# Kernel optimization log

Hardware: AMD Instinct MI355X
Metric: run time of the kernel (lower is better)

## Reference

```python
import jax, jax.numpy as jnp
import numpy as np
import math

HEADS = 32
DIM_HEAD = 64
DM = HEADS * DIM_HEAD  # 2048
B, S = 2, 1024
BITS = 3
N_LEVELS = 2 ** BITS
N_GROUPS = (DIM_HEAD + 2) // 3  # 22
PAD = (3 - DIM_HEAD % 3) % 3    # 2
EPS_NORM = 1e-8
EPS_RMS = 1e-6


def _rotors_to_matrices(r):
    # r: (G,4) unit rotors [s, b12, b13, b23] -> (G,3,3) rotation matrices
    s, p, q, rr = r[:, 0], r[:, 1], r[:, 2], r[:, 3]
    s2, p2, q2, r2 = s * s, p * p, q * q, rr * rr
    M = np.zeros((r.shape[0], 3, 3), dtype=np.float32)
    M[:, 0, 0] = s2 - p2 - q2 + r2
    M[:, 0, 1] = 2 * s * p - 2 * q * rr
    M[:, 0, 2] = 2 * s * q + 2 * p * rr
    M[:, 1, 0] = -2 * s * p - 2 * q * rr
    M[:, 1, 1] = s2 - p2 + q2 - r2
    M[:, 1, 2] = 2 * s * rr - 2 * p * q
    M[:, 2, 0] = -2 * s * q + 2 * p * rr
    M[:, 2, 1] = -2 * s * rr - 2 * p * q
    M[:, 2, 2] = s2 + p2 - q2 - r2
    return M


def _make_compressor(seed):
    rng = np.random.default_rng(seed)
    rot = rng.standard_normal((N_GROUPS, 4)).astype(np.float32)
    rot /= np.linalg.norm(rot, axis=-1, keepdims=True)
    M = _rotors_to_matrices(rot)
    sigma = 1.0 / math.sqrt(DIM_HEAD)  # Lloyd-Max for N(0, 1/d)
    C = np.linspace(-3 * sigma, 3 * sigma, N_LEVELS, dtype=np.float32)
    return jnp.asarray(M), jnp.asarray(np.ascontiguousarray(M.transpose(0, 2, 1))), jnp.asarray(C)


def setup_inputs() -> dict:
    key = jax.random.key(0)
    ks = jax.random.split(key, 8)
    x = jax.random.normal(ks[0], (B, S, DM), dtype=jnp.float32)
    w_scale = 0.02
    Wq = jax.random.normal(ks[1], (DM, DM), dtype=jnp.float32) * w_scale
    Wk = jax.random.normal(ks[2], (DM, DM), dtype=jnp.float32) * w_scale
    Wv = jax.random.normal(ks[3], (DM, DM), dtype=jnp.float32) * w_scale
    Wo = jax.random.normal(ks[4], (DM, DM), dtype=jnp.float32) * w_scale
    qn_w = jnp.ones((DM,), dtype=jnp.float32)
    kn_w = jnp.ones((DM,), dtype=jnp.float32)
    Mk, Mtk, Ck = _make_compressor(42)
    Mv, Mtv, Cv = _make_compressor(4200)
    return {"x": x, "Wq": Wq, "Wk": Wk, "Wv": Wv, "Wo": Wo,
            "qn_w": qn_w, "kn_w": kn_w,
            "Mk": Mk, "Mtk": Mtk, "Ck": Ck,
            "Mv": Mv, "Mtv": Mtv, "Cv": Cv}


def _rmsnorm(x, w):
    return x * jax.lax.rsqrt(jnp.mean(x * x, axis=-1, keepdims=True) + EPS_RMS) * w


def _quant_roundtrip(h, M, Mt, C):
    """RotorQuant compress+decompress. h: (B,H,S,Dh) -> (B,H,S,Dh)."""
    norms = jnp.maximum(jnp.linalg.norm(h, axis=-1, keepdims=True), EPS_NORM)
    xu = h / norms
    xu = jnp.pad(xu, ((0, 0), (0, 0), (0, 0), (0, PAD)))
    g = xu.reshape(h.shape[0], h.shape[1], h.shape[2], N_GROUPS, 3)
    rot = jnp.einsum('bhsgi,gij->bhsgj', g, M)
    flat = rot.reshape(h.shape[0], h.shape[1], h.shape[2], N_GROUPS * 3)
    # nearest-centroid quantization (uint8 indices in original)
    idx = jnp.argmin(jnp.abs(flat[..., None] - C), axis=-1)
    deq = C[idx]
    g2 = deq.reshape(h.shape[0], h.shape[1], h.shape[2], N_GROUPS, 3)
    der = jnp.einsum('bhsgi,gij->bhsgj', g2, Mt)
    out = der.reshape(h.shape[0], h.shape[1], h.shape[2], N_GROUPS * 3)[..., :DIM_HEAD]
    return out * norms


def reference(x, Wq, Wk, Wv, Wo, qn_w, kn_w, Mk, Mtk, Ck, Mv, Mtv, Cv):
    b, s, _ = x.shape
    v = x @ Wv
    q = _rmsnorm(x @ Wq, qn_w)
    k = _rmsnorm(x @ Wk, kn_w)
    # split heads -> (B,H,S,Dh)
    qh = q.reshape(b, s, HEADS, DIM_HEAD).transpose(0, 2, 1, 3)
    kh = k.reshape(b, s, HEADS, DIM_HEAD).transpose(0, 2, 1, 3)
    vh = v.reshape(b, s, HEADS, DIM_HEAD).transpose(0, 2, 1, 3)
    # per-head rotor quantization roundtrip of K and V
    kh = _quant_roundtrip(kh, Mk, Mtk, Ck)
    vh = _quant_roundtrip(vh, Mv, Mtv, Cv)
    # scaled dot-product attention
    scores = jnp.einsum('bhqd,bhkd->bhqk', qh, kh) / math.sqrt(DIM_HEAD)
    probs = jax.nn.softmax(scores, axis=-1)
    o = jnp.einsum('bhqk,bhkd->bhqd', probs, vh)
    o = o.transpose(0, 2, 1, 3).reshape(b, s, DM)
    return o @ Wo
```

## Files before the change

### kernel.cpp

```cpp
#include <hip/hip_runtime.h>
#include <hip/hip_bf16.h>
#include <math.h>

#define HEADS 32
#define DIM_HEAD 64
#define DM 2048
#define BATCH 2
#define SEQ 1024
#define NROWS (BATCH * SEQ)
#define NVEC (NROWS * HEADS)
#define N_GROUPS 22
#define N_LEVELS 8
#define EPS_NORM 1e-8f
#define EPS_RMS 1e-6f

typedef float f32x4 __attribute__((ext_vector_type(4)));
typedef __bf16 bf16x8 __attribute__((ext_vector_type(8)));
typedef unsigned short u16x8 __attribute__((ext_vector_type(8)));
typedef unsigned short u16x4 __attribute__((ext_vector_type(4)));

__device__ __forceinline__ unsigned short f2bf(float x) {
  union { float f; unsigned u; } v; v.f = x;
  unsigned r = v.u + 0x7fffu + ((v.u >> 16) & 1u);
  return (unsigned short)(r >> 16);
}
__device__ __forceinline__ float bf2f(unsigned short h) {
  union { unsigned u; float f; } v; v.u = ((unsigned)h) << 16;
  return v.f;
}
__device__ __forceinline__ bf16x8 ldfrag(const unsigned short* p) {
  return __builtin_bit_cast(bf16x8, *(const u16x8*)p);
}
#define MFMA16(a, b, c) __builtin_amdgcn_mfma_f32_16x16x32_bf16((a), (b), (c), 0, 0, 0)

__device__ __forceinline__ void stage16(const unsigned short* g, unsigned short* lds) {
  __builtin_amdgcn_global_load_lds(
      (const __attribute__((address_space(1))) unsigned int*)g,
      (__attribute__((address_space(3))) unsigned int*)lds, 16, 0, 0);
}

#define WAITV(N) asm volatile("s_waitcnt vmcnt(" #N ")" ::: "memory")
#define SBARM()  asm volatile("s_barrier" ::: "memory")
#define SFENCE() __builtin_amdgcn_sched_barrier(0)

__global__ __launch_bounds__(256) void split_convert_kernel(
    const float* __restrict__ X, unsigned short* __restrict__ hi,
    unsigned short* __restrict__ lo, int n8) {
  const int i = blockIdx.x * 256 + threadIdx.x;
  if (i >= n8) return;
  const float4 a = ((const float4*)X)[2 * i];
  const float4 b = ((const float4*)X)[2 * i + 1];
  const float v[8] = {a.x, a.y, a.z, a.w, b.x, b.y, b.z, b.w};
  u16x8 h, l;
#pragma unroll
  for (int j = 0; j < 8; ++j) {
    const unsigned short hh = f2bf(v[j]);
    h[j] = hh;
    l[j] = f2bf(v[j] - bf2f(hh));
  }
  ((u16x8*)hi)[i] = h;
  if (lo) ((u16x8*)lo)[i] = l;
}

__global__ __launch_bounds__(256) void transpose_split_batch_kernel(
    const float* __restrict__ W0, const float* __restrict__ W1,
    const float* __restrict__ W2, const float* __restrict__ W3,
    unsigned short* __restrict__ T0h, unsigned short* __restrict__ T1h,
    unsigned short* __restrict__ T1l, unsigned short* __restrict__ T2h,
    unsigned short* __restrict__ T2l, unsigned short* __restrict__ T3h) {
  const int z = blockIdx.z;
  const float* W = (z == 0) ? W0 : (z == 1) ? W1 : (z == 2) ? W2 : W3;
  unsigned short* Th = (z == 0) ? T0h : (z == 1) ? T1h : (z == 2) ? T2h : T3h;
  unsigned short* Tl = (z == 1) ? T1l : (z == 2) ? T2l : nullptr;

  __shared__ float S[64][65];
  const int t = threadIdx.x;
  const int tk = blockIdx.y * 64, tm = blockIdx.x * 64;
  {
    const int r = t >> 2, cs = (t & 3) * 16;
    const float* src = W + (size_t)(tk + r) * DM + tm + cs;
#pragma unroll
    for (int j = 0; j < 16; j += 4) {
      float4 v = *(const float4*)(src + j);
      S[r][cs + j] = v.x; S[r][cs + j + 1] = v.y;
      S[r][cs + j + 2] = v.z; S[r][cs + j + 3] = v.w;
    }
  }
  __syncthreads();
  const int m = t >> 2, ks = (t & 3) * 16;
  u16x8 h0, h1, l0, l1;
#pragma unroll
  for (int j = 0; j < 8; ++j) {
    const float v = S[ks + j][m];
    const unsigned short hh = f2bf(v);
    h0[j] = hh; l0[j] = f2bf(v - bf2f(hh));
  }
#pragma unroll
  for (int j = 0; j < 8; ++j) {
    const float v = S[ks + 8 + j][m];
    const unsigned short hh = f2bf(v);
    h1[j] = hh; l1[j] = f2bf(v - bf2f(hh));
  }
  const size_t o = (size_t)(tm + m) * DM + tk + ks;
  *(u16x8*)&Th[o] = h0; *(u16x8*)&Th[o + 8] = h1;
  if (Tl) { *(u16x8*)&Tl[o] = l0; *(u16x8*)&Tl[o + 8] = l1; }
}

__global__ __launch_bounds__(256) void qkv_gemm_kernel(
    const unsigned short* __restrict__ Ahi, const unsigned short* __restrict__ Alo,
    const unsigned short* __restrict__ Bhi, const unsigned short* __restrict__ Blo,
    float* __restrict__ q, float* __restrict__ k, float* __restrict__ v) {
  __shared__ unsigned short lAhi[128 * 32];
  __shared__ unsigned short lBhi[128 * 32];
  __shared__ unsigned short lAlo[128 * 32];
  __shared__ unsigned short lBlo[128 * 32];

  const int t = threadIdx.x;
  const int lane = t & 63, wave = t >> 6;
  const int wr = wave >> 1, wc = wave & 1;
  const int gm0 = blockIdx.y * 128;
  const int gnc = blockIdx.x * 128;
  const int seg = gnc >> 11;
  const bool split = (seg != 0);
  const int lrsub = lane >> 2;
  const int lcsub = lane & 3;

  f32x4 acc[4][4] = {};

  for (int kt = 0; kt < DM; kt += 32) {
    __syncthreads();
#pragma unroll
    for (int rg = wave; rg < 8; rg += 4) {
      const int lrow = rg * 16 + lrsub;
      const int c = lcsub ^ ((lrow >> 1) & 3);
      const size_t goffA = (size_t)(gm0 + lrow) * DM + kt + c * 8;
      const size_t goffB = (size_t)(gnc + lrow) * DM + kt + c * 8;
      stage16(Ahi + goffA, lAhi + rg * 512);
      stage16(Bhi + goffB, lBhi + rg * 512);
      if (split) {
        stage16(Alo + goffA, lAlo + rg * 512);
        stage16(Blo + goffB, lBlo + rg * 512);
      }
    }
    __syncthreads();

    bf16x8 ah[4], bh[4], al[4], bl[4];
#pragma unroll
    for (int i = 0; i < 4; ++i) {
      const int mrow = wr * 64 + i * 16 + (lane & 15);
      const int offa = mrow * 32 + (((lane >> 4) ^ ((mrow >> 1) & 3)) << 3);
      ah[i] = ldfrag(&lAhi[offa]);
      const int nrow = wc * 64 + i * 16 + (lane & 15);
      const int offb = nrow * 32 + (((lane >> 4) ^ ((nrow >> 1) & 3)) << 3);
      bh[i] = ldfrag(&lBhi[offb]);
      if (split) {
        al[i] = ldfrag(&lAlo[offa]);
        bl[i] = ldfrag(&lBlo[offb]);
      }
    }
#pragma unroll
    for (int i = 0; i < 4; ++i)
#pragma unroll
      for (int j = 0; j < 4; ++j) {
        acc[i][j] = MFMA16(ah[i], bh[j], acc[i][j]);
        if (split) {
          acc[i][j] = MFMA16(ah[i], bl[j], acc[i][j]);
          acc[i][j] = MFMA16(al[i], bh[j], acc[i][j]);
        }
      }
  }

  float* C = (seg == 0) ? q : (seg == 1) ? k : v;
  const int gn0 = gnc & 2047;
#pragma unroll
  for (int i = 0; i < 4; ++i) {
    const int row = gm0 + wr * 64 + i * 16 + ((lane >> 4) << 2);
#pragma unroll
    for (int j = 0; j < 4; ++j) {
      const int col = gn0 + wc * 64 + j * 16 + (lane & 15);
#pragma unroll
      for (int r = 0; r < 4; ++r)
        C[(size_t)(row + r) * DM + col] = acc[i][j][r];
    }
  }
}

__global__ __launch_bounds__(256) void gemm_out_splitk_kernel(
    const unsigned short* __restrict__ Ahi, const unsigned short* __restrict__ Bt,
    float* __restrict__ Cpart) {
  __shared__ unsigned short lAhi[128 * 32];
  __shared__ unsigned short lBhi[128 * 32];

  const int t = threadIdx.x;
  const int lane = t & 63, wave = t >> 6;
  const int wr = wave >> 1, wc = wave & 1;
  const int gm0 = blockIdx.y * 128, gn0 = blockIdx.x * 128;
  const int z = blockIdx.z;
  const int k0 = z * (DM / 2);
  const int lrsub = lane >> 2;
  const int lcsub = lane & 3;

  f32x4 acc[4][4] = {};

  for (int kt = k0; kt < k0 + DM / 2; kt += 32) {
    __syncthreads();
#pragma unroll
    for (int rg = wave; rg < 8; rg += 4) {
      const int lrow = rg * 16 + lrsub;
      const int c = lcsub ^ ((lrow >> 1) & 3);
      stage16(Ahi + (size_t)(gm0 + lrow) * DM + kt + c * 8, lAhi + rg * 512);
      stage16(Bt + (size_t)(gn0 + lrow) * DM + kt + c * 8, lBhi + rg * 512);
    }
    __syncthreads();

    bf16x8 ah[4], bh[4];
#pragma unroll
    for (int i = 0; i < 4; ++i) {
      const int mrow = wr * 64 + i * 16 + (lane & 15);
      ah[i] = ldfrag(&lAhi[mrow * 32 + (((lane >> 4) ^ ((mrow >> 1) & 3)) << 3)]);
      const int nrow = wc * 64 + i * 16 + (lane & 15);
      bh[i] = ldfrag(&lBhi[nrow * 32 + (((lane >> 4) ^ ((nrow >> 1) & 3)) << 3)]);
    }
#pragma unroll
    for (int i = 0; i < 4; ++i)
#pragma unroll
      for (int j = 0; j < 4; ++j)
        acc[i][j] = MFMA16(ah[i], bh[j], acc[i][j]);
  }

  float* C = Cpart + (size_t)z * NROWS * DM;
#pragma unroll
  for (int i = 0; i < 4; ++i) {
    const int row = gm0 + wr * 64 + i * 16 + ((lane >> 4) << 2);
#pragma unroll
    for (int j = 0; j < 4; ++j) {
      const int col = gn0 + wc * 64 + j * 16 + (lane & 15);
#pragma unroll
      for (int r = 0; r < 4; ++r)
        C[(size_t)(row + r) * DM + col] = acc[i][j][r];
    }
  }
}

__global__ __launch_bounds__(256) void add2_f4_kernel(
    const float* __restrict__ a, const float* __restrict__ b,
    float* __restrict__ o, int n4) {
  const int i = blockIdx.x * 256 + threadIdx.x;
  if (i >= n4) return;
  const float4 x = ((const float4*)a)[i];
  const float4 y = ((const float4*)b)[i];
  ((float4*)o)[i] = make_float4(x.x + y.x, x.y + y.y, x.z + y.z, x.w + y.w);
}

__device__ __forceinline__ float wave_sum(float x) {
#pragma unroll
  for (int o = 32; o > 0; o >>= 1) x += __shfl_xor(x, o, 64);
  return x;
}

__global__ __launch_bounds__(256) void rmsnorm_kernel(
    float* __restrict__ y, const float* __restrict__ w) {
  __shared__ float rbuf[4];
  const int row = blockIdx.x;
  float* p = y + (size_t)row * DM;
  const int t = threadIdx.x;
  const int wave = t >> 6, lane = t & 63;

  float ss = 0.f;
#pragma unroll
  for (int c = t; c < DM; c += 256) { float v = p[c]; ss += v * v; }
  ss = wave_sum(ss);
  if (lane == 0) rbuf[wave] = ss;
  __syncthreads();
  ss = rbuf[0] + rbuf[1] + rbuf[2] + rbuf[3];
  const float scale = rsqrtf(ss * (1.0f / DM) + EPS_RMS);
#pragma unroll
  for (int c = t; c < DM; c += 256) p[c] = p[c] * scale * w[c];
}

__global__ __launch_bounds__(256) void rmsnorm_split_kernel(
    const float* __restrict__ y, const float* __restrict__ w,
    unsigned short* __restrict__ hi, unsigned short* __restrict__ lo,
    float post) {
  __shared__ float rbuf[4];
  const int row = blockIdx.x;
  const float* p = y + (size_t)row * DM;
  const int t = threadIdx.x;
  const int wave = t >> 6, lane = t & 63;

  const int c0 = t * 8;
  float4 a = *(const float4*)(p + c0);
  float4 b = *(const float4*)(p + c0 + 4);
  float v[8] = {a.x, a.y, a.z, a.w, b.x, b.y, b.z, b.w};
  float ss = 0.f;
#pragma unroll
  for (int j = 0; j < 8; ++j) ss += v[j] * v[j];
  ss = wave_sum(ss);
  if (lane == 0) rbuf[wave] = ss;
  __syncthreads();
  ss = rbuf[0] + rbuf[1] + rbuf[2] + rbuf[3];
  const float scale = rsqrtf(ss * (1.0f / DM) + EPS_RMS) * post;

  u16x8 hv, lv;
#pragma unroll
  for (int j = 0; j < 8; ++j) {
    const float val = v[j] * scale * w[c0 + j];
    const unsigned short hh = f2bf(val);
    hv[j] = hh; lv[j] = f2bf(val - bf2f(hh));
  }
  *(u16x8*)&hi[(size_t)row * DM + c0] = hv;
  *(u16x8*)&lo[(size_t)row * DM + c0] = lv;
}

__device__ __forceinline__ float qnearest(float v, const float* __restrict__ C) {
  float best = C[0];
  float bd = fabsf(v - C[0]);
#pragma unroll
  for (int i = 1; i < N_LEVELS; ++i) {
    float d = fabsf(v - C[i]);
    if (d < bd) { bd = d; best = C[i]; }
  }
  return best;
}

template <bool WRITE_BF>
__global__ __launch_bounds__(256) void quant_kernel(
    float* __restrict__ kv, const float* __restrict__ M,
    const float* __restrict__ Mt, const float* __restrict__ C,
    unsigned short* __restrict__ hi, unsigned short* __restrict__ lo) {
  const int vec = blockIdx.x * blockDim.x + threadIdx.x;
  if (vec >= NVEC) return;
  float* p = kv + (size_t)vec * DIM_HEAD;

  float h[66];
  float ss = 0.f;
#pragma unroll
  for (int d = 0; d < DIM_HEAD; ++d) { h[d] = p[d]; ss += h[d] * h[d]; }
  float norm = fmaxf(sqrtf(ss), EPS_NORM);
  const float inv = 1.0f / norm;
#pragma unroll
  for (int d = 0; d < DIM_HEAD; ++d) h[d] *= inv;
  h[64] = 0.f; h[65] = 0.f;

#pragma unroll
  for (int g = 0; g < N_GROUPS; ++g) {
    const float* Mg  = M  + g * 9;
    const float* Mtg = Mt + g * 9;
    const float a0 = h[3 * g + 0], a1 = h[3 * g + 1], a2 = h[3 * g + 2];
    const float r0 = a0 * Mg[0] + a1 * Mg[3] + a2 * Mg[6];
    const float r1 = a0 * Mg[1] + a1 * Mg[4] + a2 * Mg[7];
    const float r2 = a0 * Mg[2] + a1 * Mg[5] + a2 * Mg[8];
    const float d0 = qnearest(r0, C);
    const float d1 = qnearest(r1, C);
    const float d2 = qnearest(r2, C);
    h[3 * g + 0] = d0 * Mtg[0] + d1 * Mtg[3] + d2 * Mtg[6];
    h[3 * g + 1] = d0 * Mtg[1] + d1 * Mtg[4] + d2 * Mtg[7];
    h[3 * g + 2] = d0 * Mtg[2] + d1 * Mtg[5] + d2 * Mtg[8];
  }
  if (WRITE_BF) {
#pragma unroll
    for (int g8 = 0; g8 < 8; ++g8) {
      u16x8 hv, lv;
#pragma unroll
      for (int j = 0; j < 8; ++j) {
        const float val = h[g8 * 8 + j] * norm;
        const unsigned short hh = f2bf(val);
        hv[j] = hh; lv[j] = f2bf(val - bf2f(hh));
      }
      *(u16x8*)&hi[(size_t)vec * DIM_HEAD + g8 * 8] = hv;
      *(u16x8*)&lo[(size_t)vec * DIM_HEAD + g8 * 8] = lv;
    }
  } else {
#pragma unroll
    for (int d = 0; d < DIM_HEAD; ++d) p[d] = h[d] * norm;
  }
}

__global__ __launch_bounds__(256) void vt_split_kernel(
    const float* __restrict__ v, unsigned short* __restrict__ hi,
    unsigned short* __restrict__ lo) {
  __shared__ float T[64][65];
  const int s0 = blockIdx.x * 64;
  const int bh = blockIdx.y;
  const int b = bh >> 5, h = bh & 31;
  const int t = threadIdx.x;
  {
    const int sr = t >> 2, dseg = (t & 3) * 16;
    const float* src = v + ((size_t)(b * SEQ + s0 + sr) * DM + h * 64 + dseg);
#pragma unroll
    for (int j = 0; j < 16; j += 4) {
      float4 a = *(const float4*)(src + j);
      T[sr][dseg + j] = a.x; T[sr][dseg + j + 1] = a.y;
      T[sr][dseg + j + 2] = a.z; T[sr][dseg + j + 3] = a.w;
    }
  }
  __syncthreads();
  const int d = t >> 2, sseg = (t & 3) * 16;
  u16x8 h0, h1, l0, l1;
#pragma unroll
  for (int j = 0; j < 8; ++j) {
    const float val = T[sseg + j][d];
    const unsigned short hh = f2bf(val);
    h0[j] = hh; l0[j] = f2bf(val - bf2f(hh));
  }
#pragma unroll
  for (int j = 0; j < 8; ++j) {
    const float val = T[sseg + 8 + j][d];
    const unsigned short hh = f2bf(val);
    h1[j] = hh; l1[j] = f2bf(val - bf2f(hh));
  }
  const size_t o = (size_t)(bh * 64 + d) * SEQ + s0 + sseg;
  *(u16x8*)&hi[o] = h0; *(u16x8*)&hi[o + 8] = h1;
  *(u16x8*)&lo[o] = l0; *(u16x8*)&lo[o + 8] = l1;
}

__global__ __launch_bounds__(256) void attn_mfma_kernel(
    const unsigned short* __restrict__ qhi, const unsigned short* __restrict__ qlo,
    const unsigned short* __restrict__ khi, const unsigned short* __restrict__ klo,
    const unsigned short* __restrict__ vthi, const unsigned short* __restrict__ vtlo,
    unsigned short* __restrict__ ohi) {
  __shared__ unsigned short Ks_h[2][4096], Ks_l[2][4096];
  __shared__ unsigned short Vt_h[2][4096], Vt_l[2][4096];
  __shared__ unsigned int   Ps[4096];

  const int bh = blockIdx.x;
  const int qt = blockIdx.y;
  const int h = bh & 31, b = bh >> 5;
  const int q0 = qt * 64;
  const int t = threadIdx.x, lane = t & 63, w = t >> 6;
  const int quad = lane >> 4, l15 = lane & 15;
  const int srow = lane >> 3, schunk = lane & 7;

  auto stage = [&](const unsigned short* g, int stride, unsigned short* arr) {
#pragma unroll
    for (int it = 0; it < 2; ++it) {
      const int r = w * 16 + it * 8 + srow;
      const int c = schunk ^ (r & 7);
      stage16(g + (size_t)r * stride + c * 8, arr + (w * 16 + it * 8) * 64);
    }
  };

  const unsigned short* gkh = khi + ((size_t)(b * SEQ) * DM + h * 64);
  const unsigned short* gkl = klo + ((size_t)(b * SEQ) * DM + h * 64);
  const unsigned short* gvh = vthi + (size_t)(bh * 64) * SEQ;
  const unsigned short* gvl = vtlo + (size_t)(bh * 64) * SEQ;

  auto stageAll = [&](int kt, int buf) {
    stage(gkh + (size_t)kt * DM, DM, Ks_h[buf]);
    stage(gkl + (size_t)kt * DM, DM, Ks_l[buf]);
    stage(gvh + kt, SEQ, Vt_h[buf]);
    stage(gvl + kt, SEQ, Vt_l[buf]);
  };

  bf16x8 qh[2], ql[2];
  {
    const size_t qrow = (size_t)(b * SEQ + q0 + w * 16 + l15) * DM + h * 64;
#pragma unroll
    for (int ks = 0; ks < 2; ++ks) {
      qh[ks] = ldfrag(&qhi[qrow + ks * 32 + quad * 8]);
      ql[ks] = ldfrag(&qlo[qrow + ks * 32 + quad * 8]);
    }
  }

  f32x4 acc[4] = {};
  float m_prev[4] = {-INFINITY, -INFINITY, -INFINITY, -INFINITY};
  float lsum[4] = {0.f, 0.f, 0.f, 0.f};

  stageAll(0, 0);

  for (int tt = 0; tt < 16; ++tt) {
    const int c = tt & 1, n = c ^ 1;
    if (tt < 15) {
      stageAll((tt + 1) * 64, n);
      WAITV(8);
    } else {
      WAITV(0);
    }
    SBARM(); SFENCE();
    const unsigned short* cKh = Ks_h[c];
    const unsigned short* cKl = Ks_l[c];
    const unsigned short* cVh = Vt_h[c];
    const unsigned short* cVl = Vt_l[c];

    f32x4 s[4] = {};
    __builtin_amdgcn_s_setprio(1);
#pragma unroll
    for (int nt = 0; nt < 4; ++nt) {
#pragma unroll
      for (int ks = 0; ks < 2; ++ks) {
        const int row = nt * 16 + l15;
        const int off = row * 64 + (((quad + 4 * ks) ^ (row & 7)) << 3);
        const bf16x8 kh = ldfrag(&cKh[off]);
        const bf16x8 kl = ldfrag(&cKl[off]);
        s[nt] = MFMA16(qh[ks], kh, s[nt]);
        s[nt] = MFMA16(qh[ks], kl, s[nt]);
        s[nt] = MFMA16(ql[ks], kh, s[nt]);
      }
    }
    __builtin_amdgcn_s_setprio(0);

    float asave[4];
#pragma unroll
    for (int r = 0; r < 4; ++r) {
      float mx = fmaxf(fmaxf(s[0][r], s[1][r]), fmaxf(s[2][r], s[3][r]));
#pragma unroll
      for (int off = 1; off < 16; off <<= 1) mx = fmaxf(mx, __shfl_xor(mx, off, 64));
      const float mn = fmaxf(m_prev[r], mx);
      const float al = __expf(m_prev[r] - mn);
      float rs = 0.f;
#pragma unroll
      for (int nt = 0; nt < 4; ++nt) {
        const float e = __expf(s[nt][r] - mn);
        s[nt][r] = e; rs += e;
      }
#pragma unroll
      for (int off = 1; off < 16; off <<= 1) rs += __shfl_xor(rs, off, 64);
      lsum[r] = lsum[r] * al + rs;
      m_prev[r] = mn;
      asave[r] = al;
      const int prow = w * 16 + quad * 4 + r;
#pragma unroll
      for (int nt = 0; nt < 4; ++nt) {
        const int kk = nt * 16 + l15;
        const unsigned short hh = f2bf(s[nt][r]);
        const unsigned short ll = f2bf(s[nt][r] - bf2f(hh));
        Ps[prow * 64 + (kk ^ ((prow & 7) << 3))] =
            ((unsigned)hh << 16) | (unsigned)ll;
      }
    }

    {
      const int src = (l15 >> 2) << 4;
      const float a0 = __shfl(asave[0], src, 64);
      const float a1 = __shfl(asave[1], src, 64);
      const float a2 = __shfl(asave[2], src, 64);
      const float a3 = __shfl(asave[3], src, 64);
      const int rr = l15 & 3;
      const float alph = (rr == 0) ? a0 : (rr == 1) ? a1 : (rr == 2) ? a2 : a3;
#pragma unroll
      for (int mt = 0; mt < 4; ++mt) acc[mt] *= alph;
    }

    bf16x8 ph[2], pl[2];
#pragma unroll
    for (int ks = 0; ks < 2; ++ks) {
      const int prow = w * 16 + l15;
      const unsigned int* pp =
          &Ps[prow * 64 + ((ks * 32 + quad * 8) ^ ((prow & 7) << 3))];
      const uint4 pa = *(const uint4*)pp;
      const uint4 pb = *(const uint4*)(pp + 4);
      u16x8 hv, lv;
      const unsigned int pw[8] = {pa.x, pa.y, pa.z, pa.w, pb.x, pb.y, pb.z, pb.w};
#pragma unroll
      for (int j = 0; j < 8; ++j) {
        hv[j] = (unsigned short)(pw[j] >> 16);
        lv[j] = (unsigned short)(pw[j] & 0xffffu);
      }
      ph[ks] = __builtin_bit_cast(bf16x8, hv);
      pl[ks] = __builtin_bit_cast(bf16x8, lv);
    }

    __builtin_amdgcn_s_setprio(1);
#pragma unroll
    for (int mt = 0; mt < 4; ++mt) {
#pragma unroll
      for (int ks = 0; ks < 2; ++ks) {
        const int drow = mt * 16 + l15;
        const int offv = drow * 64 + (((quad + 4 * ks) ^ (drow & 7)) << 3);
        const bf16x8 vh = ldfrag(&cVh[offv]);
        const bf16x8 vl = ldfrag(&cVl[offv]);
        acc[mt] = MFMA16(vh, ph[ks], acc[mt]);
        acc[mt] = MFMA16(vh, pl[ks], acc[mt]);
        acc[mt] = MFMA16(vl, ph[ks], acc[mt]);
      }
    }
    __builtin_amdgcn_s_setprio(0);
    SFENCE(); SBARM();
  }

  {
    const int src = (l15 >> 2) << 4;
    const float a0 = __shfl(lsum[0], src, 64);
    const float a1 = __shfl(lsum[1], src, 64);
    const float a2 = __shfl(lsum[2], src, 64);
    const float a3 = __shfl(lsum[3], src, 64);
    const int rr = l15 & 3;
    const float lq = (rr == 0) ? a0 : (rr == 1) ? a1 : (rr == 2) ? a2 : a3;
    const float inv = 1.0f / lq;
    const size_t obase = (size_t)(b * SEQ + q0 + w * 16 + l15) * DM + h * 64;
#pragma unroll
    for (int mt = 0; mt < 4; ++mt) {
      u16x4 ov;
#pragma unroll
      for (int r = 0; r < 4; ++r) ov[r] = f2bf(acc[mt][r] * inv);
      *(u16x4*)&ohi[obase + mt * 16 + quad * 4] = ov;
    }
  }
}

extern "C" void kernel_launch(void* const* d_in, const int* in_sizes, int n_in,
                              void* d_out, int out_size, void* d_ws, size_t ws_size,
                              hipStream_t stream) {
  const float* x    = (const float*)d_in[0];
  const float* Wq   = (const float*)d_in[1];
  const float* Wk   = (const float*)d_in[2];
  const float* Wv   = (const float*)d_in[3];
  const float* Wo   = (const float*)d_in[4];
  const float* qn_w = (const float*)d_in[5];
  const float* kn_w = (const float*)d_in[6];
  const float* Mk   = (const float*)d_in[7];
  const float* Mtk  = (const float*)d_in[8];
  const float* Ck   = (const float*)d_in[9];
  const float* Mv   = (const float*)d_in[10];
  const float* Mtv  = (const float*)d_in[11];
  const float* Cv   = (const float*)d_in[12];
  float* out = (float*)d_out;

  const size_t MBb = 1024ull * 1024ull;
  const size_t SEG = (size_t)DM * DM;
  char* w = (char*)d_ws;
  float* qb = (float*)(w + 0 * MBb);
  float* kb = (float*)(w + 16 * MBb);
  float* vb = (float*)(w + 32 * MBb);
  unsigned short* xhi     = (unsigned short*)(w + 48 * MBb);
  unsigned short* xlo     = (unsigned short*)(w + 56 * MBb);
  unsigned short* wcat_hi = (unsigned short*)(w + 64 * MBb);
  unsigned short* wcat_lo = (unsigned short*)(w + 88 * MBb);
  unsigned short* wot     = (unsigned short*)(w + 112 * MBb);
  unsigned short* q_hi  = wcat_hi;
  unsigned short* k_hi  = wcat_hi + SEG;
  unsigned short* k_lo  = wcat_hi + 2 * SEG;
  unsigned short* q_lo  = wcat_lo;
  unsigned short* vt_hi = wcat_lo + SEG;
  unsigned short* vt_lo = wcat_lo + 2 * SEG;
  unsigned short* o_hi  = xhi;
  float* opart = (float*)(w + 0 * MBb);

  const int n8 = (NROWS * DM) / 8;

  split_convert_kernel<<<n8 / 256, 256, 0, stream>>>(x, xhi, xlo, n8);
  transpose_split_batch_kernel<<<dim3(DM / 64, DM / 64, 4), 256, 0, stream>>>(
      Wq, Wk, Wv, Wo,
      wcat_hi, wcat_hi + SEG, wcat_lo + SEG, wcat_hi + 2 * SEG, wcat_lo + 2 * SEG, wot);

  qkv_gemm_kernel<<<dim3(3 * DM / 128, NROWS / 128), 256, 0, stream>>>(
      xhi, xlo, wcat_hi, wcat_lo, qb, kb, vb);

  rmsnorm_kernel<<<NROWS, 256, 0, stream>>>(kb, kn_w);
  rmsnorm_split_kernel<<<NROWS, 256, 0, stream>>>(qb, qn_w, q_hi, q_lo, 0.125f);

  quant_kernel<true ><<<NVEC / 256, 256, 0, stream>>>(kb, Mk, Mtk, Ck, k_hi, k_lo);
  quant_kernel<false><<<NVEC / 256, 256, 0, stream>>>(vb, Mv, Mtv, Cv, nullptr, nullptr);
  vt_split_kernel<<<dim3(SEQ / 64, BATCH * HEADS), 256, 0, stream>>>(vb, vt_hi, vt_lo);

  attn_mfma_kernel<<<dim3(BATCH * HEADS, SEQ / 64), 256, 0, stream>>>(
      q_hi, q_lo, k_hi, k_lo, vt_hi, vt_lo, o_hi);

  gemm_out_splitk_kernel<<<dim3(DM / 128, NROWS / 128, 2), 256, 0, stream>>>(
      o_hi, wot, opart);
  add2_f4_kernel<<<(NROWS * DM / 4 + 255) / 256, 256, 0, stream>>>(
      opart, opart + (size_t)NROWS * DM, out, NROWS * DM / 4);
}
```

Measured before the change: 461.1 us.

## Split QKV GEMM into pipelined K/V split-precision and plain Q kernels

```diff
diff --git a/kernel.cpp b/kernel.cpp
--- a/kernel.cpp
+++ b/kernel.cpp
@@ -106,78 +106,99 @@
   if (Tl) { *(u16x8*)&Tl[o] = l0; *(u16x8*)&Tl[o + 8] = l1; }
 }
 
-__global__ __launch_bounds__(256) void qkv_gemm_kernel(
-    const unsigned short* __restrict__ Ahi, const unsigned short* __restrict__ Alo,
-    const unsigned short* __restrict__ Bhi, const unsigned short* __restrict__ Blo,
-    float* __restrict__ q, float* __restrict__ k, float* __restrict__ v) {
-  __shared__ unsigned short lAhi[128 * 32];
-  __shared__ unsigned short lBhi[128 * 32];
-  __shared__ unsigned short lAlo[128 * 32];
-  __shared__ unsigned short lBlo[128 * 32];
-
-  const int t = threadIdx.x;
-  const int lane = t & 63, wave = t >> 6;
+
+__global__ __launch_bounds__(256, 2) void gemm_kv3p_kernel(
+    const unsigned short* __restrict__ Ah_, const unsigned short* __restrict__ Al_,
+    const unsigned short* __restrict__ Bh_, const unsigned short* __restrict__ Bl_,
+    float* __restrict__ kout, float* __restrict__ vout) {
+  __shared__ unsigned short L[2][4][128 * 32];
+
+  const int t = threadIdx.x, lane = t & 63, wave = t >> 6;
   const int wr = wave >> 1, wc = wave & 1;
   const int gm0 = blockIdx.y * 128;
-  const int gnc = blockIdx.x * 128;
-  const int seg = gnc >> 11;
-  const bool split = (seg != 0);
-  const int lrsub = lane >> 2;
-  const int lcsub = lane & 3;
+  const int x = blockIdx.x;
+  const int seg = x >> 4;
+  const int gn0 = (x & 15) * 128;
+  const int nAbs = 2048 + x * 128;
+  const int quad = lane >> 4, l15 = lane & 15;
+  const int srow = lane >> 2, schunk = lane & 3;
+
+  auto stg = [&](const unsigned short* g, int row0, int kt, unsigned short* dst) {
+#pragma unroll
+    for (int it = 0; it < 2; ++it) {
+      const int r = (it * 4 + wave) * 16 + srow;
+      const int cg = schunk ^ ((r >> 1) & 3);
+      stage16(g + (size_t)(row0 + r) * DM + kt + cg * 8,
+              dst + ((it * 4 + wave) * 16) * 32);
+    }
+  };
 
   f32x4 acc[4][4] = {};
-
-  for (int kt = 0; kt < DM; kt += 32) {
-    __syncthreads();
-#pragma unroll
-    for (int rg = wave; rg < 8; rg += 4) {
-      const int lrow = rg * 16 + lrsub;
-      const int c = lcsub ^ ((lrow >> 1) & 3);
-      const size_t goffA = (size_t)(gm0 + lrow) * DM + kt + c * 8;
-      const size_t goffB = (size_t)(gnc + lrow) * DM + kt + c * 8;
-      stage16(Ahi + goffA, lAhi + rg * 512);
-      stage16(Bhi + goffB, lBhi + rg * 512);
-      if (split) {
-        stage16(Alo + goffA, lAlo + rg * 512);
-        stage16(Blo + goffB, lBlo + rg * 512);
-      }
-    }
-    __syncthreads();
-
-    bf16x8 ah[4], bh[4], al[4], bl[4];
+  bf16x8 ah[4], bh[4], xt[4];
+
+  auto rdA = [&](bf16x8* fr, const unsigned short* arr) {
 #pragma unroll
     for (int i = 0; i < 4; ++i) {
-      const int mrow = wr * 64 + i * 16 + (lane & 15);
-      const int offa = mrow * 32 + (((lane >> 4) ^ ((mrow >> 1) & 3)) << 3);
-      ah[i] = ldfrag(&lAhi[offa]);
-      const int nrow = wc * 64 + i * 16 + (lane & 15);
-      const int offb = nrow * 32 + (((lane >> 4) ^ ((nrow >> 1) & 3)) << 3);
-      bh[i] = ldfrag(&lBhi[offb]);
-      if (split) {
-        al[i] = ldfrag(&lAlo[offa]);
-        bl[i] = ldfrag(&lBlo[offb]);
-      }
-    }
+      const int row = wr * 64 + i * 16 + l15;
+      fr[i] = ldfrag(&arr[row * 32 + ((quad ^ ((row >> 1) & 3)) << 3)]);
+    }
+  };
+  auto rdB = [&](bf16x8* fr, const unsigned short* arr) {
+#pragma unroll
+    for (int j = 0; j < 4; ++j) {
+      const int row = wc * 64 + j * 16 + l15;
+      fr[j] = ldfrag(&arr[row * 32 + ((quad ^ ((row >> 1) & 3)) << 3)]);
+    }
+  };
+  auto mm = [&](const bf16x8* fa, const bf16x8* fb) {
+    __builtin_amdgcn_s_setprio(1);
 #pragma unroll
     for (int i = 0; i < 4; ++i)
 #pragma unroll
-      for (int j = 0; j < 4; ++j) {
-        acc[i][j] = MFMA16(ah[i], bh[j], acc[i][j]);
-        if (split) {
-          acc[i][j] = MFMA16(ah[i], bl[j], acc[i][j]);
-          acc[i][j] = MFMA16(al[i], bh[j], acc[i][j]);
-        }
-      }
-  }
-
-  float* C = (seg == 0) ? q : (seg == 1) ? k : v;
-  const int gn0 = gnc & 2047;
+      for (int j = 0; j < 4; ++j)
+        acc[i][j] = MFMA16(fa[i], fb[j], acc[i][j]);
+    __builtin_amdgcn_s_setprio(0);
+  };
+
+  stg(Ah_, gm0, 0, L[0][0]);
+  stg(Bh_, nAbs, 0, L[0][1]);
+  stg(Bl_, nAbs, 0, L[0][2]);
+  stg(Al_, gm0, 0, L[0][3]);
+
+  for (int tt = 0; tt < 64; ++tt) {
+    const int c = tt & 1, n = c ^ 1;
+    const bool pf = (tt + 1 < 64);
+    const int ktn = (tt + 1) << 5;
+
+    if (pf) { stg(Ah_, gm0, ktn, L[n][0]); stg(Bh_, nAbs, ktn, L[n][1]); WAITV(8); }
+    else WAITV(4);
+    SBARM(); SFENCE();
+    rdA(ah, L[c][0]); rdB(bh, L[c][1]);
+    mm(ah, bh);
+    SFENCE(); SBARM();
+
+    if (pf) { stg(Bl_, nAbs, ktn, L[n][2]); WAITV(8); }
+    else WAITV(2);
+    SBARM(); SFENCE();
+    rdB(xt, L[c][2]);
+    mm(ah, xt);
+    SFENCE(); SBARM();
+
+    if (pf) { stg(Al_, gm0, ktn, L[n][3]); WAITV(8); }
+    else WAITV(0);
+    SBARM(); SFENCE();
+    rdA(xt, L[c][3]);
+    mm(xt, bh);
+    SFENCE(); SBARM();
+  }
+
+  float* C = seg ? vout : kout;
 #pragma unroll
   for (int i = 0; i < 4; ++i) {
-    const int row = gm0 + wr * 64 + i * 16 + ((lane >> 4) << 2);
+    const int row = gm0 + wr * 64 + i * 16 + (quad << 2);
 #pragma unroll
     for (int j = 0; j < 4; ++j) {
-      const int col = gn0 + wc * 64 + j * 16 + (lane & 15);
+      const int col = gn0 + wc * 64 + j * 16 + l15;
 #pragma unroll
       for (int r = 0; r < 4; ++r)
         C[(size_t)(row + r) * DM + col] = acc[i][j][r];
@@ -185,59 +206,77 @@
   }
 }
 
-__global__ __launch_bounds__(256) void gemm_out_splitk_kernel(
-    const unsigned short* __restrict__ Ahi, const unsigned short* __restrict__ Bt,
-    float* __restrict__ Cpart) {
-  __shared__ unsigned short lAhi[128 * 32];
-  __shared__ unsigned short lBhi[128 * 32];
-
-  const int t = threadIdx.x;
-  const int lane = t & 63, wave = t >> 6;
+__global__ __launch_bounds__(256, 3) void gemm_plain_pipe_kernel(
+    const unsigned short* __restrict__ A, const unsigned short* __restrict__ B,
+    float* __restrict__ C, int ntiles) {
+  __shared__ unsigned short L[2][2][128 * 32];
+
+  const int t = threadIdx.x, lane = t & 63, wave = t >> 6;
   const int wr = wave >> 1, wc = wave & 1;
-  const int gm0 = blockIdx.y * 128, gn0 = blockIdx.x * 128;
-  const int z = blockIdx.z;
-  const int k0 = z * (DM / 2);
-  const int lrsub = lane >> 2;
-  const int lcsub = lane & 3;
+  const int gm0 = blockIdx.y * 128;
+  const int gn0 = blockIdx.x * 128;
+  const int k0 = blockIdx.z * (ntiles << 5);
+  const int quad = lane >> 4, l15 = lane & 15;
+  const int srow = lane >> 2, schunk = lane & 3;
+
+  auto stg = [&](const unsigned short* g, int row0, int kt, unsigned short* dst) {
+#pragma unroll
+    for (int it = 0; it < 2; ++it) {
+      const int r = (it * 4 + wave) * 16 + srow;
+      const int cg = schunk ^ ((r >> 1) & 3);
+      stage16(g + (size_t)(row0 + r) * DM + kt + cg * 8,
+              dst + ((it * 4 + wave) * 16) * 32);
+    }
+  };
 
   f32x4 acc[4][4] = {};
-
-  for (int kt = k0; kt < k0 + DM / 2; kt += 32) {
-    __syncthreads();
-#pragma unroll
-    for (int rg = wave; rg < 8; rg += 4) {
-      const int lrow = rg * 16 + lrsub;
-      const int c = lcsub ^ ((lrow >> 1) & 3);
-      stage16(Ahi + (size_t)(gm0 + lrow) * DM + kt + c * 8, lAhi + rg * 512);
-      stage16(Bt + (size_t)(gn0 + lrow) * DM + kt + c * 8, lBhi + rg * 512);
-    }
-    __syncthreads();
-
-    bf16x8 ah[4], bh[4];
+  bf16x8 fa[4], fb[4];
+
+  stg(A, gm0, k0, L[0][0]);
+  stg(B, gn0, k0, L[0][1]);
+
+  for (int tt = 0; tt < ntiles; ++tt) {
+    const int c = tt & 1, n = c ^ 1;
+    const bool pf = (tt + 1 < ntiles);
+    if (pf) {
+      const int ktn = k0 + ((tt + 1) << 5);
+      stg(A, gm0, ktn, L[n][0]);
+      stg(B, gn0, ktn, L[n][1]);
+      WAITV(4);
+    } else {
+      WAITV(0);
+    }
+    SBARM(); SFENCE();
 #pragma unroll
     for (int i = 0; i < 4; ++i) {
-      const int mrow = wr * 64 + i * 16 + (lane & 15);
-      ah[i] = ldfrag(&lAhi[mrow * 32 + (((lane >> 4) ^ ((mrow >> 1) & 3)) << 3)]);
-      const int nrow = wc * 64 + i * 16 + (lane & 15);
-      bh[i] = ldfrag(&lBhi[nrow * 32 + (((lane >> 4) ^ ((nrow >> 1) & 3)) << 3)]);
-    }
+      const int row = wr * 64 + i * 16 + l15;
+      fa[i] = ldfrag(&L[c][0][row * 32 + ((quad ^ ((row >> 1) & 3)) << 3)]);
+    }
+#pragma unroll
+    for (int j = 0; j < 4; ++j) {
+      const int row = wc * 64 + j * 16 + l15;
+      fb[j] = ldfrag(&L[c][1][row * 32 + ((quad ^ ((row >> 1) & 3)) << 3)]);
+    }
+    __builtin_amdgcn_s_setprio(1);
 #pragma unroll
     for (int i = 0; i < 4; ++i)
 #pragma unroll
       for (int j = 0; j < 4; ++j)
-        acc[i][j] = MFMA16(ah[i], bh[j], acc[i][j]);
-  }
-
-  float* C = Cpart + (size_t)z * NROWS * DM;
+        acc[i][j] = MFMA16(fa[i], fb[j], acc[i][j]);
+    __builtin_amdgcn_s_setprio(0);
+    SFENCE(); SBARM();
+  }
+
+  float* Cz = C + (size_t)blockIdx.z * NROWS * DM;
 #pragma unroll
   for (int i = 0; i < 4; ++i) {
-    const int row = gm0 + wr * 64 + i * 16 + ((lane >> 4) << 2);
+    const int row = gm0 + wr * 64 + i * 16 + (quad << 2);
 #pragma unroll
     for (int j = 0; j < 4; ++j) {
-      const int col = gn0 + wc * 64 + j * 16 + (lane & 15);
+      const int col = gn0 + wc * 64 + j * 16 + l15;
 #pragma unroll
       for (int r = 0; r < 4; ++r)
-        C[(size_t)(row + r) * DM + col] = acc[i][j][r];
+        Cz[(size_t)(row + r) * DM + col] = acc[i][j][r];
     }
   }
 }
@@ -643,8 +682,10 @@
       Wq, Wk, Wv, Wo,
       wcat_hi, wcat_hi + SEG, wcat_lo + SEG, wcat_hi + 2 * SEG, wcat_lo + 2 * SEG, wot);
 
-  qkv_gemm_kernel<<<dim3(3 * DM / 128, NROWS / 128), 256, 0, stream>>>(
-      xhi, xlo, wcat_hi, wcat_lo, qb, kb, vb);
+  gemm_kv3p_kernel<<<dim3(32, 16), 256, 0, stream>>>(
+      xhi, xlo, wcat_hi, wcat_lo, kb, vb);
+  gemm_plain_pipe_kernel<<<dim3(16, 16, 1), 256, 0, stream>>>(
+      xhi, wcat_hi, qb, 64);
 
   rmsnorm_kernel<<<NROWS, 256, 0, stream>>>(kb, kn_w);
   rmsnorm_split_kernel<<<NROWS, 256, 0, stream>>>(qb, qn_w, q_hi, q_lo, 0.125f);
@@ -656,8 +697,8 @@
   attn_mfma_kernel<<<dim3(BATCH * HEADS, SEQ / 64), 256, 0, stream>>>(
       q_hi, q_lo, k_hi, k_lo, vt_hi, vt_lo, o_hi);
 
-  gemm_out_splitk_kernel<<<dim3(DM / 128, NROWS / 128, 2), 256, 0, stream>>>(
-      o_hi, wot, opart);
+  gemm_plain_pipe_kernel<<<dim3(16, 16, 2), 256, 0, stream>>>(
+      o_hi, wot, opart, 32);
   add2_f4_kernel<<<(NROWS * DM / 4 + 255) / 256, 256, 0, stream>>>(
       opart, opart + (size_t)NROWS * DM, out, NROWS * DM / 4);
 }
```

Measured after the change: 474.8 us. +3.0%, slower.

## Transpose QK^T MFMA output so softmax rows live per lane, use exp2

Applied to the files above, without the earlier changes.

```diff
diff --git a/kernel.cpp b/kernel.cpp
--- a/kernel.cpp
+++ b/kernel.cpp
@@ -18,6 +18,12 @@
 typedef __bf16 bf16x8 __attribute__((ext_vector_type(8)));
 typedef unsigned short u16x8 __attribute__((ext_vector_type(8)));
 typedef unsigned short u16x4 __attribute__((ext_vector_type(4)));
+
+#if __has_builtin(__builtin_amdgcn_exp2f)
+#define EXP2F(x) __builtin_amdgcn_exp2f(x)
+#else
+#define EXP2F(x) exp2f(x)
+#endif
 
 __device__ __forceinline__ unsigned short f2bf(float x) {
   union { float f; unsigned u; } v; v.f = x;
@@ -430,6 +436,8 @@
   const int t = threadIdx.x, lane = t & 63, w = t >> 6;
   const int quad = lane >> 4, l15 = lane & 15;
   const int srow = lane >> 3, schunk = lane & 7;
+  const int pswz = (l15 & 7) << 2;
+  unsigned int* Psw = Ps + w * 1024;
 
   auto stage = [&](const unsigned short* g, int stride, unsigned short* arr) {
 #pragma unroll
@@ -463,8 +471,8 @@
   }
 
   f32x4 acc[4] = {};
-  float m_prev[4] = {-INFINITY, -INFINITY, -INFINITY, -INFINITY};
-  float lsum[4] = {0.f, 0.f, 0.f, 0.f};
+  float m_prev = -INFINITY;
+  float lsum = 0.f;
 
   stageAll(0, 0);
 
@@ -492,63 +500,58 @@
         const int off = row * 64 + (((quad + 4 * ks) ^ (row & 7)) << 3);
         const bf16x8 kh = ldfrag(&cKh[off]);
         const bf16x8 kl = ldfrag(&cKl[off]);
-        s[nt] = MFMA16(qh[ks], kh, s[nt]);
-        s[nt] = MFMA16(qh[ks], kl, s[nt]);
-        s[nt] = MFMA16(ql[ks], kh, s[nt]);
+        s[nt] = MFMA16(kh, qh[ks], s[nt]);
+        s[nt] = MFMA16(kl, qh[ks], s[nt]);
+        s[nt] = MFMA16(kh, ql[ks], s[nt]);
       }
     }
     __builtin_amdgcn_s_setprio(0);
 
-    float asave[4];
-#pragma unroll
-    for (int r = 0; r < 4; ++r) {
-      float mx = fmaxf(fmaxf(s[0][r], s[1][r]), fmaxf(s[2][r], s[3][r]));
-#pragma unroll
-      for (int off = 1; off < 16; off <<= 1) mx = fmaxf(mx, __shfl_xor(mx, off, 64));
-      const float mn = fmaxf(m_prev[r], mx);
-      const float al = __expf(m_prev[r] - mn);
-      float rs = 0.f;
-#pragma unroll
-      for (int nt = 0; nt < 4; ++nt) {
-        const float e = __expf(s[nt][r] - mn);
+    float mx = s[0][0];
+#pragma unroll
+    for (int nt = 0; nt < 4; ++nt)
+#pragma unroll
+      for (int r = 0; r < 4; ++r) mx = fmaxf(mx, s[nt][r]);
+    mx = fmaxf(mx, __shfl_xor(mx, 16, 64));
+    mx = fmaxf(mx, __shfl_xor(mx, 32, 64));
+    const float mn = fmaxf(m_prev, mx);
+    const float al = EXP2F(m_prev - mn);
+    float rs = 0.f;
+#pragma unroll
+    for (int nt = 0; nt < 4; ++nt)
+#pragma unroll
+      for (int r = 0; r < 4; ++r) {
+        const float e = EXP2F(s[nt][r] - mn);
         s[nt][r] = e; rs += e;
       }
-#pragma unroll
-      for (int off = 1; off < 16; off <<= 1) rs += __shfl_xor(rs, off, 64);
-      lsum[r] = lsum[r] * al + rs;
-      m_prev[r] = mn;
-      asave[r] = al;
-      const int prow = w * 16 + quad * 4 + r;
-#pragma unroll
-      for (int nt = 0; nt < 4; ++nt) {
-        const int kk = nt * 16 + l15;
+    rs += __shfl_xor(rs, 16, 64);
+    rs += __shfl_xor(rs, 32, 64);
+    lsum = lsum * al + rs;
+    m_prev = mn;
+#pragma unroll
+    for (int mt = 0; mt < 4; ++mt) acc[mt] *= al;
+
+#pragma unroll
+    for (int nt = 0; nt < 4; ++nt) {
+      uint4 pw;
+      unsigned int* wp = (unsigned int*)&pw;
+#pragma unroll
+      for (int r = 0; r < 4; ++r) {
         const unsigned short hh = f2bf(s[nt][r]);
         const unsigned short ll = f2bf(s[nt][r] - bf2f(hh));
-        Ps[prow * 64 + (kk ^ ((prow & 7) << 3))] =
-            ((unsigned)hh << 16) | (unsigned)ll;
-      }
-    }
-
-    {
-      const int src = (l15 >> 2) << 4;
-      const float a0 = __shfl(asave[0], src, 64);
-      const float a1 = __shfl(asave[1], src, 64);
-      const float a2 = __shfl(asave[2], src, 64);
-      const float a3 = __shfl(asave[3], src, 64);
-      const int rr = l15 & 3;
-      const float alph = (rr == 0) ? a0 : (rr == 1) ? a1 : (rr == 2) ? a2 : a3;
-#pragma unroll
-      for (int mt = 0; mt < 4; ++mt) acc[mt] *= alph;
+        wp[r] = ((unsigned)hh << 16) | (unsigned)ll;
+      }
+      const int cb = (nt * 16 + quad * 4) ^ pswz;
+      *(uint4*)&Psw[l15 * 64 + cb] = pw;
     }
 
     bf16x8 ph[2], pl[2];
 #pragma unroll
     for (int ks = 0; ks < 2; ++ks) {
-      const int prow = w * 16 + l15;
-      const unsigned int* pp =
-          &Ps[prow * 64 + ((ks * 32 + quad * 8) ^ ((prow & 7) << 3))];
-      const uint4 pa = *(const uint4*)pp;
-      const uint4 pb = *(const uint4*)(pp + 4);
+      const int c0 = (ks * 32 + quad * 8) ^ pswz;
+      const int c1 = (ks * 32 + quad * 8 + 4) ^ pswz;
+      const uint4 pa = *(const uint4*)&Psw[l15 * 64 + c0];
+      const uint4 pb = *(const uint4*)&Psw[l15 * 64 + c1];
       u16x8 hv, lv;
       const unsigned int pw[8] = {pa.x, pa.y, pa.z, pa.w, pb.x, pb.y, pb.z, pb.w};
 #pragma unroll
@@ -579,14 +582,7 @@
   }
 
   {
-    const int src = (l15 >> 2) << 4;
-    const float a0 = __shfl(lsum[0], src, 64);
-    const float a1 = __shfl(lsum[1], src, 64);
-    const float a2 = __shfl(lsum[2], src, 64);
-    const float a3 = __shfl(lsum[3], src, 64);
-    const int rr = l15 & 3;
-    const float lq = (rr == 0) ? a0 : (rr == 1) ? a1 : (rr == 2) ? a2 : a3;
-    const float inv = 1.0f / lq;
+    const float inv = 1.0f / lsum;
     const size_t obase = (size_t)(b * SEQ + q0 + w * 16 + l15) * DM + h * 64;
 #pragma unroll
     for (int mt = 0; mt < 4; ++mt) {
@@ -647,7 +643,8 @@
       xhi, xlo, wcat_hi, wcat_lo, qb, kb, vb);
 
   rmsnorm_kernel<<<NROWS, 256, 0, stream>>>(kb, kn_w);
-  rmsnorm_split_kernel<<<NROWS, 256, 0, stream>>>(qb, qn_w, q_hi, q_lo, 0.125f);
+  rmsnorm_split_kernel<<<NROWS, 256, 0, stream>>>(
+      qb, qn_w, q_hi, q_lo, 0.125f * 1.4426950408889634f);
 
   quant_kernel<true ><<<NVEC / 256, 256, 0, stream>>>(kb, Mk, Mtk, Ck, k_hi, k_lo);
   quant_kernel<false><<<NVEC / 256, 256, 0, stream>>>(vb, Mv, Mtv, Cv, nullptr, nullptr);
```

Result: faster. 440.9 us (-4.4%).
